# Kernel optimization log

Hardware: AMD Instinct MI355X
Metric: run time of the kernel (lower is better)

Reference implementation:

```python
import jax, jax.numpy as jnp
import numpy as np

B, K, D = 8, 2048, 1024

def setup_inputs() -> dict:
    key = jax.random.key(0)
    k1, k2 = jax.random.split(key)
    x = jax.random.normal(k1, (B, K, D), dtype=jnp.float32)
    W = jax.random.normal(k2, (K, K), dtype=jnp.float32) * 0.02  # dt_proj weight [out=K, in=K]
    b = jnp.zeros((K,), dtype=jnp.float32)                        # dt_proj bias
    return {"x": x, "W": W, "b": b}

def _scan_combine(c1, c2):
    # compose affine maps s -> a*s + u; (a1,u1) then (a2,u2)
    a1, u1 = c1
    a2, u2 = c2
    return (a2 * a1, a2 * u1 + u2)

def reference(x, W, b):
    # lam[b,t,d] = sigmoid( sum_k x[b,k,d] * W[t,k] + b[t] )
    # (dt_proj is a Linear over the TIME axis after permute(0,2,1))
    lam = jax.nn.sigmoid(jnp.einsum('bkd,tk->btd', x, W) + b[None, :, None])
    # s_t = lam_t * s_{t-1} + (1 - lam_t) * x_t, s_0 = 0  -> associative scan over time
    _, ys = jax.lax.associative_scan(_scan_combine, (lam, (1.0 - lam) * x), axis=1)
    return ys
```

## Files before the change

### kernel.cpp

```cpp
#include <hip/hip_runtime.h>
#include <hip/hip_bf16.h>
#include <stdint.h>

#define B_ 8
#define K_ 2048
#define D_ 1024
#define NC 32
#define TC (K_ / NC)

typedef float v4f __attribute__((ext_vector_type(4)));
typedef short v8s __attribute__((ext_vector_type(8)));

__device__ __forceinline__ unsigned short f2bf(float f) {
    __hip_bfloat16 h = __float2bfloat16(f);
    return *reinterpret_cast<unsigned short*>(&h);
}

__device__ __forceinline__ void async_ld16(const void* g, void* l) {
    __builtin_amdgcn_global_load_lds(
        (__attribute__((address_space(1))) void*)(void*)g,
        (__attribute__((address_space(3))) void*)l,
        16, 0, 0);
}

__global__ void conv_w(const float* __restrict__ W, unsigned short* __restrict__ Wb) {
    int i = (blockIdx.x * 256 + threadIdx.x) * 4;
    float4 v = *(const float4*)(W + i);
    ushort4 o;
    o.x = f2bf(v.x); o.y = f2bf(v.y); o.z = f2bf(v.z); o.w = f2bf(v.w);
    *(ushort4*)(Wb + i) = o;
}

__global__ void conv_x_t(const float* __restrict__ x, unsigned short* __restrict__ xT) {
    const int k0 = blockIdx.x * 64, d0 = blockIdx.y * 64, bb = blockIdx.z;
    __shared__ unsigned short tile[64][68];
    const int tid = threadIdx.x;
    const int tx = tid & 15, ty = tid >> 4;
    const float* xp = x + (size_t)bb * K_ * D_;
#pragma unroll
    for (int r = 0; r < 4; r++) {
        int row = ty + r * 16;
        float4 v = *(const float4*)(xp + (size_t)(k0 + row) * D_ + d0 + tx * 4);
        tile[row][tx * 4 + 0] = f2bf(v.x);
        tile[row][tx * 4 + 1] = f2bf(v.y);
        tile[row][tx * 4 + 2] = f2bf(v.z);
        tile[row][tx * 4 + 3] = f2bf(v.w);
    }
    __syncthreads();
    unsigned short* op = xT + (size_t)bb * D_ * K_;
#pragma unroll
    for (int r = 0; r < 4; r++) {
        int dcol = ty + r * 16;
        ushort4 u;
        u.x = tile[tx * 4 + 0][dcol];
        u.y = tile[tx * 4 + 1][dcol];
        u.z = tile[tx * 4 + 2][dcol];
        u.w = tile[tx * 4 + 3][dcol];
        *(ushort4*)(op + (size_t)(d0 + dcol) * K_ + k0 + tx * 4) = u;
    }
}

__launch_bounds__(512, 2)
__global__ void gemm_sig(const unsigned short* __restrict__ Wb,
                         const unsigned short* __restrict__ xT,
                         const float* __restrict__ bias,
                         const float* __restrict__ xf,
                         float* __restrict__ lam,
                         float* __restrict__ Ac,
                         float* __restrict__ Uc,
                         int fuse) {
    __shared__ __align__(16) unsigned short smem_all[2][2][2][256 * 32];

    const int bid = blockIdx.x;
    const int lid = (bid & 7) * 32 + (bid >> 3);
    const int bb = lid >> 5;
    const int tM = (lid >> 2) & 7;
    const int tN = lid & 3;

    const int tid = threadIdx.x;
    const int w = tid >> 6;
    const int lane = tid & 63;
    const int wm = w >> 2;
    const int wn = w & 3;
    const int quad = lane >> 4;
    const int l16 = lane & 15;

    const unsigned short* Ag = Wb + (size_t)(tM * 256) * K_;
    const unsigned short* Bg = xT + (size_t)bb * D_ * K_ + (size_t)(tN * 256) * K_;

    const int srow = lane >> 2;
    const int sgk8 = ((lane & 3) ^ ((lane >> 3) & 3)) * 8;

    const int frg = (quad ^ ((l16 >> 1) & 3)) * 8;
    const int aoff = (wm * 128 + l16) * 32 + frg;
    const int boff = (wn * 64 + l16) * 32 + frg;

    v4f acc[8][4];
#pragma unroll
    for (int i = 0; i < 8; i++)
#pragma unroll
        for (int j = 0; j < 4; j++) acc[i][j] = (v4f)0.f;

#define STAGE_(op, bufi, kh, kk, Gp)                                                        \
    do {                                                                                    \
        async_ld16(Gp + (size_t)(w * 16 + srow) * K_ + (kk) + (kh) * 32 + sgk8,             \
                   &smem_all[op][bufi][kh][w * 512]);                                       \
        async_ld16(Gp + (size_t)((8 + w) * 16 + srow) * K_ + (kk) + (kh) * 32 + sgk8,       \
                   &smem_all[op][bufi][kh][(8 + w) * 512]);                                 \
    } while (0)

    STAGE_(0, 0, 0, 0, Ag);
    STAGE_(1, 0, 0, 0, Bg);
    STAGE_(0, 0, 1, 0, Ag);
    STAGE_(1, 0, 1, 0, Bg);
    asm volatile("s_waitcnt vmcnt(4)");
    asm volatile("s_barrier" ::: "memory");

    v8s af[8], bf[2];

    for (int t = 0; t < K_ / 64; ++t) {
        const int cur = t & 1, nxt = cur ^ 1;
        int k1 = (t + 1) * 64;
        if (k1 == K_) k1 = 0;

#pragma unroll
        for (int i = 0; i < 8; i++) af[i] = *(const v8s*)(&smem_all[0][cur][0][aoff + i * 512]);
        bf[0] = *(const v8s*)(&smem_all[1][cur][0][boff]);
        bf[1] = *(const v8s*)(&smem_all[1][cur][0][boff + 512]);
        STAGE_(0, nxt, 0, k1, Ag);
        asm volatile("s_barrier" ::: "memory");
        asm volatile("s_waitcnt lgkmcnt(0)");
        __builtin_amdgcn_sched_barrier(0);
        __builtin_amdgcn_s_setprio(1);
#pragma unroll
        for (int i = 0; i < 8; i++) {
            acc[i][0] = __builtin_amdgcn_mfma_f32_16x16x32_bf16(af[i], bf[0], acc[i][0], 0, 0, 0);
            acc[i][1] = __builtin_amdgcn_mfma_f32_16x16x32_bf16(af[i], bf[1], acc[i][1], 0, 0, 0);
        }
        __builtin_amdgcn_s_setprio(0);
        asm volatile("s_barrier" ::: "memory");

        bf[0] = *(const v8s*)(&smem_all[1][cur][0][boff + 2 * 512]);
        bf[1] = *(const v8s*)(&smem_all[1][cur][0][boff + 3 * 512]);
        STAGE_(1, nxt, 0, k1, Bg);
        asm volatile("s_barrier" ::: "memory");
        asm volatile("s_waitcnt lgkmcnt(0)");
        __builtin_amdgcn_sched_barrier(0);
        __builtin_amdgcn_s_setprio(1);
#pragma unroll
        for (int i = 0; i < 8; i++) {
            acc[i][2] = __builtin_amdgcn_mfma_f32_16x16x32_bf16(af[i], bf[0], acc[i][2], 0, 0, 0);
            acc[i][3] = __builtin_amdgcn_mfma_f32_16x16x32_bf16(af[i], bf[1], acc[i][3], 0, 0, 0);
        }
        __builtin_amdgcn_s_setprio(0);
        asm volatile("s_waitcnt vmcnt(4)");
        asm volatile("s_barrier" ::: "memory");

#pragma unroll
        for (int i = 0; i < 8; i++) af[i] = *(const v8s*)(&smem_all[0][cur][1][aoff + i * 512]);
        bf[0] = *(const v8s*)(&smem_all[1][cur][1][boff]);
        bf[1] = *(const v8s*)(&smem_all[1][cur][1][boff + 512]);
        STAGE_(0, nxt, 1, k1, Ag);
        asm volatile("s_barrier" ::: "memory");
        asm volatile("s_waitcnt lgkmcnt(0)");
        __builtin_amdgcn_sched_barrier(0);
        __builtin_amdgcn_s_setprio(1);
#pragma unroll
        for (int i = 0; i < 8; i++) {
            acc[i][0] = __builtin_amdgcn_mfma_f32_16x16x32_bf16(af[i], bf[0], acc[i][0], 0, 0, 0);
            acc[i][1] = __builtin_amdgcn_mfma_f32_16x16x32_bf16(af[i], bf[1], acc[i][1], 0, 0, 0);
        }
        __builtin_amdgcn_s_setprio(0);
        asm volatile("s_barrier" ::: "memory");

        bf[0] = *(const v8s*)(&smem_all[1][cur][1][boff + 2 * 512]);
        bf[1] = *(const v8s*)(&smem_all[1][cur][1][boff + 3 * 512]);
        STAGE_(1, nxt, 1, k1, Bg);
        asm volatile("s_barrier" ::: "memory");
        asm volatile("s_waitcnt lgkmcnt(0)");
        __builtin_amdgcn_sched_barrier(0);
        __builtin_amdgcn_s_setprio(1);
#pragma unroll
        for (int i = 0; i < 8; i++) {
            acc[i][2] = __builtin_amdgcn_mfma_f32_16x16x32_bf16(af[i], bf[0], acc[i][2], 0, 0, 0);
            acc[i][3] = __builtin_amdgcn_mfma_f32_16x16x32_bf16(af[i], bf[1], acc[i][3], 0, 0, 0);
        }
        __builtin_amdgcn_s_setprio(0);
        asm volatile("s_waitcnt vmcnt(4)");
        asm volatile("s_barrier" ::: "memory");
    }
#undef STAGE_

    asm volatile("s_waitcnt vmcnt(0)");
    asm volatile("s_barrier" ::: "memory");

    float* out = lam + (size_t)bb * K_ * D_;
    const int dg = tN * 256 + wn * 64;

    if (fuse) {
        float* Swp = (float*)smem_all + w * 4096;
        const int swzw = quad * 16;
#pragma unroll
        for (int cg = 0; cg < 2; cg++) {
            const int c = tM * 4 + wm * 2 + cg;
            const int t0 = c * 64;
#pragma unroll
            for (int ii = 0; ii < 4; ii++) {
                int i = cg * 4 + ii;
                int rowb = t0 + ii * 16 + quad * 4;
                int Rb = ii * 16 + quad * 4;
#pragma unroll
                for (int r = 0; r < 4; r++) {
                    float bt = bias[rowb + r];
#pragma unroll
                    for (int j = 0; j < 4; j++) {
                        int colc = j * 16 + l16;
                        float v = acc[i][j][r] + bt;
                        float sg = 1.f / (1.f + __expf(-v));
                        out[(size_t)(rowb + r) * D_ + dg + colc] = sg;
                        Swp[(Rb + r) * 64 + (colc ^ swzw)] = sg;
                    }
                }
            }
            asm volatile("s_waitcnt lgkmcnt(0)");
            __builtin_amdgcn_sched_barrier(0);
            const float* xg = xf + ((size_t)bb * K_ + t0) * D_ + dg + lane;
            float A = 1.f, U = 0.f;
#pragma unroll 8
            for (int tt = 0; tt < 64; tt++) {
                float l = Swp[tt * 64 + (lane ^ (((tt >> 2) & 3) * 16))];
                float xv = xg[(size_t)tt * D_];
                A *= l;
                U = l * U + (1.f - l) * xv;
            }
            size_t oi = ((size_t)bb * NC + c) * D_ + dg + lane;
            Ac[oi] = A;
            Uc[oi] = U;
            __builtin_amdgcn_sched_barrier(0);
        }
    } else {
#pragma unroll
        for (int i = 0; i < 8; i++) {
            int rowb = tM * 256 + wm * 128 + i * 16 + quad * 4;
#pragma unroll
            for (int r = 0; r < 4; r++) {
                float bt = bias[rowb + r];
#pragma unroll
                for (int j = 0; j < 4; j++) {
                    int col = tN * 256 + wn * 64 + j * 16 + l16;
                    float v = acc[i][j][r] + bt;
                    out[(size_t)(rowb + r) * D_ + col] = 1.f / (1.f + __expf(-v));
                }
            }
        }
    }
}

__global__ void scan_pass1(const float* __restrict__ lam, const float* __restrict__ x,
                           float* __restrict__ Ac, float* __restrict__ Uc) {
    int id = blockIdx.x * 256 + threadIdx.x;
    int d2 = (id & 511) * 2;
    int c = (id >> 9) & (NC - 1);
    int bb = id >> 14;
    const float* lp = lam + ((size_t)bb * K_ + (size_t)c * TC) * D_ + d2;
    const float* xp = x   + ((size_t)bb * K_ + (size_t)c * TC) * D_ + d2;
    float2 A = make_float2(1.f, 1.f), U = make_float2(0.f, 0.f);
#pragma unroll 8
    for (int t = 0; t < TC; t++) {
        float2 l  = *(const float2*)(lp + (size_t)t * D_);
        float2 xv = *(const float2*)(xp + (size_t)t * D_);
        A.x *= l.x; A.y *= l.y;
        U.x = l.x * U.x + (1.f - l.x) * xv.x;
        U.y = l.y * U.y + (1.f - l.y) * xv.y;
    }
    size_t oi = ((size_t)bb * NC + c) * D_ + d2;
    *(float2*)(Ac + oi) = A;
    *(float2*)(Uc + oi) = U;
}

__global__ void scan_pass2(const float* __restrict__ Ac, const float* __restrict__ Uc,
                           float* __restrict__ Sin) {
    int id = blockIdx.x * 64 + threadIdx.x;
    int d = id & (D_ - 1);
    int bb = id >> 10;
    float s = 0.f;
#pragma unroll
    for (int c = 0; c < NC; c++) {
        int idx = (bb * NC + c) * D_ + d;
        Sin[idx] = s;
        s = Ac[idx] * s + Uc[idx];
    }
}

__global__ void scan_pass3(const float* __restrict__ x, const float* __restrict__ Sin,
                           float* __restrict__ lamout) {
    int id = blockIdx.x * 256 + threadIdx.x;
    int d2 = (id & 511) * 2;
    int c = (id >> 9) & (NC - 1);
    int bb = id >> 14;
    float* lp = lamout + ((size_t)bb * K_ + (size_t)c * TC) * D_ + d2;
    const float* xp = x + ((size_t)bb * K_ + (size_t)c * TC) * D_ + d2;
    size_t si = ((size_t)bb * NC + c) * D_ + d2;
    float2 s = *(const float2*)(Sin + si);
#pragma unroll 8
    for (int t = 0; t < TC; t++) {
        float2 l  = *(const float2*)(lp + (size_t)t * D_);
        float2 xv = *(const float2*)(xp + (size_t)t * D_);
        s.x = l.x * s.x + (1.f - l.x) * xv.x;
        s.y = l.y * s.y + (1.f - l.y) * xv.y;
        *(float2*)(lp + (size_t)t * D_) = s;
    }
}

extern "C" void kernel_launch(void* const* d_in, const int* in_sizes, int n_in,
                              void* d_out, int out_size, void* d_ws, size_t ws_size,
                              hipStream_t stream) {
    const float* x    = (const float*)d_in[0];
    const float* W    = (const float*)d_in[1];
    const float* bias = (const float*)d_in[2];
    float* out = (float*)d_out;
    char* ws = (char*)d_ws;

    unsigned short* xT = (unsigned short*)ws;
    unsigned short* Wb = (unsigned short*)(ws + 33554432);

    const int fuse = (ws_size >= 44040192u) ? 1 : 0;
    float* Ac, * Uc;
    if (fuse) {
        Ac = (float*)(ws + 41943040);
        Uc = (float*)(ws + 41943040 + 1048576);
    } else {
        Ac = (float*)(ws + 33554432);
        Uc = (float*)(ws + 33554432 + 1048576);
    }
    float* Sin = (float*)(ws + 33554432 + 2097152);

    conv_w<<<dim3(K_ * K_ / 4 / 256), 256, 0, stream>>>(W, Wb);
    conv_x_t<<<dim3(K_ / 64, D_ / 64, B_), 256, 0, stream>>>(x, xT);
    gemm_sig<<<dim3(256), dim3(512), 0, stream>>>(Wb, xT, bias, x, out, Ac, Uc, fuse);
    if (!fuse)
        scan_pass1<<<dim3(B_ * NC * D_ / 2 / 256), 256, 0, stream>>>(out, x, Ac, Uc);
    scan_pass2<<<dim3(B_ * D_ / 64), 64, 0, stream>>>(Ac, Uc, Sin);
    scan_pass3<<<dim3(B_ * NC * D_ / 2 / 256), 256, 0, stream>>>(x, Sin, out);
}
```

Baseline: 237.5 us.

## Fuse conversion kernels, triple-buffer GEMM pipeline, fold scan pass2 into pass3

Merges the W and x-transpose conversion kernels into one launch. Restructures the GEMM main loop into 32-wide K halves with a 4-slot ring buffer, keeping three stages in flight instead of double buffering. Removes scan_pass2: each pass3 thread recomputes its chunk's carry-in serially from the chunk summaries. Pass3 now writes its output with nontemporal stores. The trade is some redundant carry arithmetic per thread and deeper vmcnt waits in exchange for fewer launches and more load latency hiding.

```diff
diff --git a/kernel.cpp b/kernel.cpp
--- a/kernel.cpp
+++ b/kernel.cpp
@@ -23,16 +23,18 @@
         16, 0, 0);
 }
 
-__global__ void conv_w(const float* __restrict__ W, unsigned short* __restrict__ Wb) {
-    int i = (blockIdx.x * 256 + threadIdx.x) * 4;
-    float4 v = *(const float4*)(W + i);
-    ushort4 o;
-    o.x = f2bf(v.x); o.y = f2bf(v.y); o.z = f2bf(v.z); o.w = f2bf(v.w);
-    *(ushort4*)(Wb + i) = o;
-}
-
-__global__ void conv_x_t(const float* __restrict__ x, unsigned short* __restrict__ xT) {
-    const int k0 = blockIdx.x * 64, d0 = blockIdx.y * 64, bb = blockIdx.z;
+__global__ void conv_all(const float* __restrict__ W, unsigned short* __restrict__ Wb,
+                         const float* __restrict__ x, unsigned short* __restrict__ xT) {
+    if (blockIdx.x < 4096) {
+        int i = (blockIdx.x * 256 + threadIdx.x) * 4;
+        float4 v = *(const float4*)(W + i);
+        ushort4 o;
+        o.x = f2bf(v.x); o.y = f2bf(v.y); o.z = f2bf(v.z); o.w = f2bf(v.w);
+        *(ushort4*)(Wb + i) = o;
+        return;
+    }
+    const int t = blockIdx.x - 4096;
+    const int k0 = (t & 31) * 64, d0 = ((t >> 5) & 15) * 64, bb = t >> 9;
     __shared__ unsigned short tile[64][68];
     const int tid = threadIdx.x;
     const int tx = tid & 15, ty = tid >> 4;
@@ -69,7 +71,7 @@
                          float* __restrict__ Ac,
                          float* __restrict__ Uc,
                          int fuse) {
-    __shared__ __align__(16) unsigned short smem_all[2][2][2][256 * 32];
+    __shared__ __align__(16) unsigned short smem_all[2][4][256 * 32];
 
     const int bid = blockIdx.x;
     const int lid = (bid & 7) * 32 + (bid >> 3);
@@ -101,98 +103,81 @@
 #pragma unroll
         for (int j = 0; j < 4; j++) acc[i][j] = (v4f)0.f;
 
-#define STAGE_(op, bufi, kh, kk, Gp)                                                        \
+#define STAGE_A_(hh)                                                                        \
     do {                                                                                    \
-        async_ld16(Gp + (size_t)(w * 16 + srow) * K_ + (kk) + (kh) * 32 + sgk8,             \
-                   &smem_all[op][bufi][kh][w * 512]);                                       \
-        async_ld16(Gp + (size_t)((8 + w) * 16 + srow) * K_ + (kk) + (kh) * 32 + sgk8,       \
-                   &smem_all[op][bufi][kh][(8 + w) * 512]);                                 \
+        const int slot_ = (hh) & 3; const int ko_ = (hh) * 32;                              \
+        async_ld16(Ag + (size_t)(w * 16 + srow) * K_ + ko_ + sgk8,                          \
+                   &smem_all[0][slot_][w * 512]);                                           \
+        async_ld16(Ag + (size_t)((8 + w) * 16 + srow) * K_ + ko_ + sgk8,                    \
+                   &smem_all[0][slot_][(8 + w) * 512]);                                     \
     } while (0)
-
-    STAGE_(0, 0, 0, 0, Ag);
-    STAGE_(1, 0, 0, 0, Bg);
-    STAGE_(0, 0, 1, 0, Ag);
-    STAGE_(1, 0, 1, 0, Bg);
-    asm volatile("s_waitcnt vmcnt(4)");
+#define STAGE_B_(hh)                                                                        \
+    do {                                                                                    \
+        const int slot_ = (hh) & 3; const int ko_ = (hh) * 32;                              \
+        async_ld16(Bg + (size_t)(w * 16 + srow) * K_ + ko_ + sgk8,                          \
+                   &smem_all[1][slot_][w * 512]);                                           \
+        async_ld16(Bg + (size_t)((8 + w) * 16 + srow) * K_ + ko_ + sgk8,                    \
+                   &smem_all[1][slot_][(8 + w) * 512]);                                     \
+    } while (0)
+
+    v8s af[8], bf[2];
+
+#define HALF_(hh, DO_STAGE, VM_)                                                            \
+    do {                                                                                    \
+        const int s_ = (hh) & 3;                                                            \
+        const unsigned short* As_ = &smem_all[0][s_][0];                                    \
+        const unsigned short* Bs_ = &smem_all[1][s_][0];                                    \
+                                                                   \
+        _Pragma("unroll")                                                                   \
+        for (int i = 0; i < 8; i++) af[i] = *(const v8s*)(&As_[aoff + i * 512]);            \
+        bf[0] = *(const v8s*)(&Bs_[boff]);                                                  \
+        bf[1] = *(const v8s*)(&Bs_[boff + 512]);                                            \
+        if (DO_STAGE) STAGE_A_((hh) + 3);                                                   \
+        asm volatile("s_barrier" ::: "memory");                                             \
+        asm volatile("s_waitcnt lgkmcnt(0)");                                               \
+        __builtin_amdgcn_sched_barrier(0);                                                  \
+        __builtin_amdgcn_s_setprio(1);                                                      \
+        _Pragma("unroll")                                                                   \
+        for (int i = 0; i < 8; i++) {                                                       \
+            acc[i][0] = __builtin_amdgcn_mfma_f32_16x16x32_bf16(af[i], bf[0], acc[i][0], 0, 0, 0); \
+            acc[i][1] = __builtin_amdgcn_mfma_f32_16x16x32_bf16(af[i], bf[1], acc[i][1], 0, 0, 0); \
+        }                                                                                   \
+        __builtin_amdgcn_s_setprio(0);                                                      \
+        asm volatile("s_barrier" ::: "memory");                                             \
+                                                                   \
+        bf[0] = *(const v8s*)(&Bs_[boff + 2 * 512]);                                        \
+        bf[1] = *(const v8s*)(&Bs_[boff + 3 * 512]);                                        \
+        if (DO_STAGE) STAGE_B_((hh) + 3);                                                   \
+        asm volatile("s_barrier" ::: "memory");                                             \
+        asm volatile("s_waitcnt lgkmcnt(0)");                                               \
+        __builtin_amdgcn_sched_barrier(0);                                                  \
+        __builtin_amdgcn_s_setprio(1);                                                      \
+        _Pragma("unroll")                                                                   \
+        for (int i = 0; i < 8; i++) {                                                       \
+            acc[i][2] = __builtin_amdgcn_mfma_f32_16x16x32_bf16(af[i], bf[0], acc[i][2], 0, 0, 0); \
+            acc[i][3] = __builtin_amdgcn_mfma_f32_16x16x32_bf16(af[i], bf[1], acc[i][3], 0, 0, 0); \
+        }                                                                                   \
+        __builtin_amdgcn_s_setprio(0);                                                      \
+        VM_;                                                                                \
+        asm volatile("s_barrier" ::: "memory");                                             \
+    } while (0)
+
+    STAGE_A_(0); STAGE_B_(0);
+    STAGE_A_(1); STAGE_B_(1);
+    STAGE_A_(2); STAGE_B_(2);
+    asm volatile("s_waitcnt vmcnt(8)");
     asm volatile("s_barrier" ::: "memory");
 
-    v8s af[8], bf[2];
-
-    for (int t = 0; t < K_ / 64; ++t) {
-        const int cur = t & 1, nxt = cur ^ 1;
-        int k1 = (t + 1) * 64;
-        if (k1 == K_) k1 = 0;
-
-#pragma unroll
-        for (int i = 0; i < 8; i++) af[i] = *(const v8s*)(&smem_all[0][cur][0][aoff + i * 512]);
-        bf[0] = *(const v8s*)(&smem_all[1][cur][0][boff]);
-        bf[1] = *(const v8s*)(&smem_all[1][cur][0][boff + 512]);
-        STAGE_(0, nxt, 0, k1, Ag);
-        asm volatile("s_barrier" ::: "memory");
-        asm volatile("s_waitcnt lgkmcnt(0)");
-        __builtin_amdgcn_sched_barrier(0);
-        __builtin_amdgcn_s_setprio(1);
-#pragma unroll
-        for (int i = 0; i < 8; i++) {
-            acc[i][0] = __builtin_amdgcn_mfma_f32_16x16x32_bf16(af[i], bf[0], acc[i][0], 0, 0, 0);
-            acc[i][1] = __builtin_amdgcn_mfma_f32_16x16x32_bf16(af[i], bf[1], acc[i][1], 0, 0, 0);
-        }
-        __builtin_amdgcn_s_setprio(0);
-        asm volatile("s_barrier" ::: "memory");
-
-        bf[0] = *(const v8s*)(&smem_all[1][cur][0][boff + 2 * 512]);
-        bf[1] = *(const v8s*)(&smem_all[1][cur][0][boff + 3 * 512]);
-        STAGE_(1, nxt, 0, k1, Bg);
-        asm volatile("s_barrier" ::: "memory");
-        asm volatile("s_waitcnt lgkmcnt(0)");
-        __builtin_amdgcn_sched_barrier(0);
-        __builtin_amdgcn_s_setprio(1);
-#pragma unroll
-        for (int i = 0; i < 8; i++) {
-            acc[i][2] = __builtin_amdgcn_mfma_f32_16x16x32_bf16(af[i], bf[0], acc[i][2], 0, 0, 0);
-            acc[i][3] = __builtin_amdgcn_mfma_f32_16x16x32_bf16(af[i], bf[1], acc[i][3], 0, 0, 0);
-        }
-        __builtin_amdgcn_s_setprio(0);
-        asm volatile("s_waitcnt vmcnt(4)");
-        asm volatile("s_barrier" ::: "memory");
-
-#pragma unroll
-        for (int i = 0; i < 8; i++) af[i] = *(const v8s*)(&smem_all[0][cur][1][aoff + i * 512]);
-        bf[0] = *(const v8s*)(&smem_all[1][cur][1][boff]);
-        bf[1] = *(const v8s*)(&smem_all[1][cur][1][boff + 512]);
-        STAGE_(0, nxt, 1, k1, Ag);
-        asm volatile("s_barrier" ::: "memory");
-        asm volatile("s_waitcnt lgkmcnt(0)");
-        __builtin_amdgcn_sched_barrier(0);
-        __builtin_amdgcn_s_setprio(1);
-#pragma unroll
-        for (int i = 0; i < 8; i++) {
-            acc[i][0] = __builtin_amdgcn_mfma_f32_16x16x32_bf16(af[i], bf[0], acc[i][0], 0, 0, 0);
-            acc[i][1] = __builtin_amdgcn_mfma_f32_16x16x32_bf16(af[i], bf[1], acc[i][1], 0, 0, 0);
-        }
-        __builtin_amdgcn_s_setprio(0);
-        asm volatile("s_barrier" ::: "memory");
-
-        bf[0] = *(const v8s*)(&smem_all[1][cur][1][boff + 2 * 512]);
-        bf[1] = *(const v8s*)(&smem_all[1][cur][1][boff + 3 * 512]);
-        STAGE_(1, nxt, 1, k1, Bg);
-        asm volatile("s_barrier" ::: "memory");
-        asm volatile("s_waitcnt lgkmcnt(0)");
-        __builtin_amdgcn_sched_barrier(0);
-        __builtin_amdgcn_s_setprio(1);
-#pragma unroll
-        for (int i = 0; i < 8; i++) {
-            acc[i][2] = __builtin_amdgcn_mfma_f32_16x16x32_bf16(af[i], bf[0], acc[i][2], 0, 0, 0);
-            acc[i][3] = __builtin_amdgcn_mfma_f32_16x16x32_bf16(af[i], bf[1], acc[i][3], 0, 0, 0);
-        }
-        __builtin_amdgcn_s_setprio(0);
-        asm volatile("s_waitcnt vmcnt(4)");
-        asm volatile("s_barrier" ::: "memory");
-    }
-#undef STAGE_
-
-    asm volatile("s_waitcnt vmcnt(0)");
-    asm volatile("s_barrier" ::: "memory");
+    const int H = K_ / 32;
+    for (int h = 0; h < H - 3; ++h)
+        HALF_(h, 1, asm volatile("s_waitcnt vmcnt(8)"));
+    HALF_(H - 3, 0, asm volatile("s_waitcnt vmcnt(4)"));
+    HALF_(H - 2, 0, asm volatile("s_waitcnt vmcnt(0)"));
+    HALF_(H - 1, 0, (void)0);
+#undef HALF_
+#undef STAGE_A_
+#undef STAGE_B_
+
 
     float* out = lam + (size_t)bb * K_ * D_;
     const int dg = tN * 256 + wn * 64;
@@ -278,37 +263,32 @@
     *(float2*)(Uc + oi) = U;
 }
 
-__global__ void scan_pass2(const float* __restrict__ Ac, const float* __restrict__ Uc,
-                           float* __restrict__ Sin) {
-    int id = blockIdx.x * 64 + threadIdx.x;
-    int d = id & (D_ - 1);
-    int bb = id >> 10;
-    float s = 0.f;
-#pragma unroll
-    for (int c = 0; c < NC; c++) {
-        int idx = (bb * NC + c) * D_ + d;
-        Sin[idx] = s;
-        s = Ac[idx] * s + Uc[idx];
-    }
-}
-
-__global__ void scan_pass3(const float* __restrict__ x, const float* __restrict__ Sin,
+__launch_bounds__(256)
+__global__ void scan_pass3(const float* __restrict__ x,
+                           const float* __restrict__ Ac, const float* __restrict__ Uc,
                            float* __restrict__ lamout) {
     int id = blockIdx.x * 256 + threadIdx.x;
-    int d2 = (id & 511) * 2;
+    int d = (id & 511) * 2;
     int c = (id >> 9) & (NC - 1);
     int bb = id >> 14;
-    float* lp = lamout + ((size_t)bb * K_ + (size_t)c * TC) * D_ + d2;
-    const float* xp = x + ((size_t)bb * K_ + (size_t)c * TC) * D_ + d2;
-    size_t si = ((size_t)bb * NC + c) * D_ + d2;
-    float2 s = *(const float2*)(Sin + si);
+    float2 s = make_float2(0.f, 0.f);
+    for (int j = 0; j < c; j++) {
+        size_t ji = ((size_t)bb * NC + j) * D_ + d;
+        float2 A = *(const float2*)(Ac + ji);
+        float2 U = *(const float2*)(Uc + ji);
+        s.x = A.x * s.x + U.x;
+        s.y = A.y * s.y + U.y;
+    }
+    float* lp = lamout + ((size_t)bb * K_ + (size_t)c * TC) * D_ + d;
+    const float* xp = x + ((size_t)bb * K_ + (size_t)c * TC) * D_ + d;
 #pragma unroll 8
     for (int t = 0; t < TC; t++) {
         float2 l  = *(const float2*)(lp + (size_t)t * D_);
         float2 xv = *(const float2*)(xp + (size_t)t * D_);
         s.x = l.x * s.x + (1.f - l.x) * xv.x;
         s.y = l.y * s.y + (1.f - l.y) * xv.y;
-        *(float2*)(lp + (size_t)t * D_) = s;
+        __builtin_nontemporal_store(s.x, lp + (size_t)t * D_);
+        __builtin_nontemporal_store(s.y, lp + (size_t)t * D_ + 1);
     }
 }
 
@@ -333,13 +313,10 @@
         Ac = (float*)(ws + 33554432);
         Uc = (float*)(ws + 33554432 + 1048576);
     }
-    float* Sin = (float*)(ws + 33554432 + 2097152);
-
-    conv_w<<<dim3(K_ * K_ / 4 / 256), 256, 0, stream>>>(W, Wb);
-    conv_x_t<<<dim3(K_ / 64, D_ / 64, B_), 256, 0, stream>>>(x, xT);
+
+    conv_all<<<dim3(8192), 256, 0, stream>>>(W, Wb, x, xT);
     gemm_sig<<<dim3(256), dim3(512), 0, stream>>>(Wb, xT, bias, x, out, Ac, Uc, fuse);
     if (!fuse)
         scan_pass1<<<dim3(B_ * NC * D_ / 2 / 256), 256, 0, stream>>>(out, x, Ac, Uc);
-    scan_pass2<<<dim3(B_ * D_ / 64), 64, 0, stream>>>(Ac, Uc, Sin);
-    scan_pass3<<<dim3(B_ * NC * D_ / 2 / 256), 256, 0, stream>>>(x, Sin, out);
-}
+    scan_pass3<<<dim3(B_ * NC * D_ / 2 / 256), 256, 0, stream>>>(x, Ac, Uc, out);
+}
```

New measurement: 237.2 us. Within noise of the previous version (-0.1%).
